# Kernel tuning notes

Measured on AMD Instinct MI355X. Metric: run time of the kernel, lower is better.

## Reference

```python
import jax, jax.numpy as jnp
import numpy as np

B, T, D, H = 4, 2048, 1024, 16
DK = D // H


def setup_inputs() -> dict:
    key = jax.random.key(0)
    ks = jax.random.split(key, 9)
    s = 1.0 / np.sqrt(D)
    x = jax.random.normal(ks[0], (B, T, D), dtype=jnp.float32)
    mask = jnp.tril(jnp.ones((T, T), dtype=bool))[None, None]  # causal [1,1,T,T]
    wq = jax.random.uniform(ks[1], (D, D), jnp.float32, -s, s)
    bq = jax.random.uniform(ks[2], (D,), jnp.float32, -s, s)
    wk = jax.random.uniform(ks[3], (D, D), jnp.float32, -s, s)
    bk = jax.random.uniform(ks[4], (D,), jnp.float32, -s, s)
    wv = jax.random.uniform(ks[5], (D, D), jnp.float32, -s, s)
    bv = jax.random.uniform(ks[6], (D,), jnp.float32, -s, s)
    wo = jax.random.uniform(ks[7], (D, D), jnp.float32, -s, s)
    bo = jax.random.uniform(ks[8], (D,), jnp.float32, -s, s)
    return {"x": x, "mask": mask, "wq": wq, "bq": bq, "wk": wk, "bk": bk,
            "wv": wv, "bv": bv, "wo": wo, "bo": bo}


def reference(x, mask, wq, bq, wk, bk, wv, bv, wo, bo):
    # projections: torch Linear is x @ W.T + b; here weights stored as (D, D) used directly
    q = (x @ wq + bq).reshape(B, T, H, DK).transpose(0, 2, 1, 3)  # [B,H,T,dk]
    k = (x @ wk + bk).reshape(B, T, H, DK).transpose(0, 2, 1, 3)
    v = (x @ wv + bv).reshape(B, T, H, DK).transpose(0, 2, 1, 3)
    scores = jnp.einsum('bhqd,bhkd->bhqk', q, k) / jnp.sqrt(jnp.float32(DK))
    scores = jnp.where(mask, scores, -jnp.inf)
    attn = jax.nn.softmax(scores, axis=-1)
    # dropout p=0.0 -> identity
    y = jnp.einsum('bhqk,bhkd->bhqd', attn, v)
    y = y.transpose(0, 2, 1, 3).reshape(B, T, D)
    return y @ wo + bo
```

## Files before the change

### kernel.cpp

```cpp
#include <hip/hip_runtime.h>


typedef short s16x8 __attribute__((ext_vector_type(8)));
typedef short s16x4 __attribute__((ext_vector_type(4)));
typedef float f32x4 __attribute__((ext_vector_type(4)));
typedef unsigned int u32x2 __attribute__((ext_vector_type(2)));

static __device__ __forceinline__ float bf2f(unsigned short u) {
    return __uint_as_float(((unsigned int)u) << 16);
}
static __device__ __forceinline__ unsigned short f2bf(float f) {
    unsigned int x = __float_as_uint(f);
    unsigned int r = x + 0x7fffu + ((x >> 16) & 1u);
    return (unsigned short)(r >> 16);
}

static __device__ __forceinline__ void gload_lds16(const short* g, short* l) {
    __builtin_amdgcn_global_load_lds((__attribute__((address_space(1))) void*)g,
                                     (__attribute__((address_space(3))) void*)l, 16, 0, 0);
}

static __device__ __forceinline__ unsigned int cvt_pk_bf16(float a, float b) {
    unsigned int r;
    asm("v_cvt_pk_bf16_f32 %0, %1, %2" : "=v"(r) : "v"(a), "v"(b));
    return r;
}

static __device__ __forceinline__ float fexp2(float x) {
    float r;
    asm("v_exp_f32 %0, %1" : "=v"(r) : "v"(x));
    return r;
}

__global__ __launch_bounds__(64) void detect_dtype(const unsigned short* __restrict__ x,
                                                   int* __restrict__ flag) {
    int lane = threadIdx.x;
    int cnt = 0;
    for (int i = 0; i < 64; ++i) {
        float v = bf2f(x[lane * 64 + i]);
        if (!(fabsf(v) < 1e10f)) cnt++;
    }
    unsigned long long m = __ballot(cnt > 0);
    if (lane == 0) *flag = (m != 0ull) ? 1 : 0;
}

__global__ __launch_bounds__(256) void convert_bf16(const void* __restrict__ src,
                                                    unsigned short* __restrict__ dst,
                                                    int n, const int* __restrict__ flag) {
    int i = blockIdx.x * 256 + threadIdx.x;
    if (i >= n) return;
    if (*flag) dst[i] = f2bf(((const float*)src)[i]);
    else       dst[i] = ((const unsigned short*)src)[i];
}

__global__ __launch_bounds__(256) void convert_biases(const void* __restrict__ b0,
                                                      const void* __restrict__ b1,
                                                      const void* __restrict__ b2,
                                                      const void* __restrict__ b3,
                                                      unsigned short* __restrict__ dst,
                                                      const int* __restrict__ flag) {
    int i = blockIdx.x * 256 + threadIdx.x;
    const void* src = (i < 1024) ? b0 : (i < 2048 ? b1 : (i < 3072 ? b2 : b3));
    int k = i & 1023;
    if (*flag) dst[i] = f2bf(((const float*)src)[k]);
    else       dst[i] = ((const unsigned short*)src)[k];
}

__global__ __launch_bounds__(256) void transpose_wt4(const void* __restrict__ s0,
                                                     const void* __restrict__ s1,
                                                     const void* __restrict__ s2,
                                                     const void* __restrict__ s3,
                                                     unsigned short* __restrict__ dst,
                                                     const int* __restrict__ flag) {
    __shared__ unsigned short t[32][33];
    int z = blockIdx.z;
    const void* src = (z == 0) ? s0 : (z == 1 ? s1 : (z == 2 ? s2 : s3));
    dst += (size_t)z * 1024 * 1024;
    int f = *flag;
    int x = threadIdx.x, y = threadIdx.y;
    int n0 = blockIdx.x * 32, k0 = blockIdx.y * 32;
    for (int j = 0; j < 32; j += 8) {
        size_t idx = (size_t)(k0 + y + j) * 1024 + n0 + x;
        t[y + j][x] = f ? f2bf(((const float*)src)[idx]) : ((const unsigned short*)src)[idx];
    }
    __syncthreads();
    for (int j = 0; j < 32; j += 8) dst[(size_t)(n0 + y + j) * 1024 + k0 + x] = t[x][y + j];
}

__global__ __launch_bounds__(256) void gemm_bf16(const short* __restrict__ A,
                                                 const short* __restrict__ Bt,
                                                 void* __restrict__ C,
                                                 short* __restrict__ vt,
                                                 const unsigned short* __restrict__ bq,
                                                 const unsigned short* __restrict__ bk,
                                                 const unsigned short* __restrict__ bv,
                                                 int K, int ldc,
                                                 const int* __restrict__ flag, int f32out,
                                                 int scale_q, int fuse_v) {
    __shared__ __align__(16) short As[2][128][64];
    __shared__ __align__(16) short Bs[2][128][64];
    int tid = threadIdx.x;
    int wid = tid >> 6, lane = tid & 63, quad = lane >> 4, l16 = lane & 15;
    int wm = wid & 1, wn = wid >> 1;
    int m0 = blockIdx.x * 128, n0 = blockIdx.y * 128;
    bool wf = f32out && (*flag != 0);

    int srow = lane >> 3;
    int schunk = (lane & 7) ^ srow;
    const short* Ag = A  + (size_t)(m0 + wid * 32 + srow) * K + schunk * 8;
    const short* Bg = Bt + (size_t)(n0 + wid * 32 + srow) * K + schunk * 8;

    f32x4 acc[4][4] = {};
    int nt = K >> 6;

#pragma unroll
    for (int c = 0; c < 4; ++c) {
        gload_lds16(Ag + c * 8 * K, &As[0][wid * 32 + c * 8][0]);
        gload_lds16(Bg + c * 8 * K, &Bs[0][wid * 32 + c * 8][0]);
    }
    __syncthreads();

    for (int t = 0; t < nt; ++t) {
        if (t + 1 < nt) {
            int bu = (t + 1) & 1;
            int kof = (t + 1) * 64;
#pragma unroll
            for (int c = 0; c < 4; ++c) {
                gload_lds16(Ag + kof + c * 8 * K, &As[bu][wid * 32 + c * 8][0]);
                gload_lds16(Bg + kof + c * 8 * K, &Bs[bu][wid * 32 + c * 8][0]);
            }
        }
        const short (*Ab)[64] = As[t & 1];
#pragma unroll
        for (int kk = 0; kk < 2; ++kk) {
            s16x8 a[4], b[4];
#pragma unroll
            for (int i = 0; i < 4; ++i) {
                int row = wm * 64 + i * 16 + l16;
                a[i] = *(const s16x8*)&Ab[row][(((kk << 2) + quad) ^ (row & 7)) << 3];
            }
#pragma unroll
            for (int j = 0; j < 4; ++j) {
                int row = wn * 64 + j * 16 + l16;
                b[j] = *(const s16x8*)&Bs[t & 1][row][(((kk << 2) + quad) ^ (row & 7)) << 3];
            }
            __builtin_amdgcn_s_setprio(1);
#pragma unroll
            for (int i = 0; i < 4; ++i)
#pragma unroll
                for (int j = 0; j < 4; ++j)
                    acc[i][j] = __builtin_amdgcn_mfma_f32_16x16x32_bf16(a[i], b[j], acc[i][j], 0, 0, 0);
            __builtin_amdgcn_s_setprio(0);
        }
        __syncthreads();
    }
    for (int j = 0; j < 4; ++j) {
        int col = n0 + wn * 64 + j * 16 + l16;
        const unsigned short* bptr = (col < 1024) ? bq : (col < 2048 ? bk : bv);
        float bias = bf2f(bptr[col & 1023]);
        float cs = (scale_q && col < 1024) ? 0.18033688f : 1.0f;
        for (int i = 0; i < 4; ++i) {
            int rbase = m0 + wm * 64 + i * 16 + quad * 4;
            if (fuse_v && col >= 2048) {
                int h = (col - 2048) >> 6, dk = col & 63;
                int bb_ = rbase >> 11, t = rbase & 2047;
                s16x4 pk;
                for (int r = 0; r < 4; ++r) pk[r] = (short)f2bf(acc[i][j][r] + bias);
                *(s16x4*)(vt + ((size_t)((bb_ * 16 + h) * 64 + dk)) * 2048 + t) = pk;
            } else {
                for (int r = 0; r < 4; ++r) {
                    float v = (acc[i][j][r] + bias) * cs;
                    size_t idx = (size_t)(rbase + r) * ldc + col;
                    if (wf) ((float*)C)[idx] = v;
                    else    ((unsigned short*)C)[idx] = f2bf(v);
                }
            }
        }
    }
}

static __device__ __forceinline__ void stage_tiles(const short* kbase, const short* vbase,
                                                   int kt, short* Kb, short* Vb,
                                                   int wid, int lane) {
    int row = wid * 8 + (lane >> 3);
    int c_src = (lane & 7) ^ (lane >> 3);
    const short* kg = kbase + (size_t)(kt * 64 + row) * 3072 + c_src * 8;
    const short* vg = vbase + (size_t)row * 2048 + kt * 64 + c_src * 8;
    gload_lds16(kg, Kb + wid * 512);
    gload_lds16(vg, Vb + wid * 512);
}

static __device__ __forceinline__ s16x8 lds_frag(const short* buf, int row, int cg) {
    int slot = cg ^ (row & 7);
    return *(const s16x8*)(buf + row * 64 + slot * 8);
}

__global__ __launch_bounds__(512, 4) void attn(const short* __restrict__ qkv,
                                               const short* __restrict__ vt,
                                               unsigned short* __restrict__ y) {
    __shared__ __align__(16) short Kbuf[3][64 * 64];
    __shared__ __align__(16) short Vbuf[3][64 * 64];
    __shared__ __align__(16) short Ps[8][16 * 68];
    int tid = threadIdx.x;
    int wid = tid >> 6, lane = tid & 63, quad = lane >> 4, l16 = lane & 15;
    int bh = blockIdx.x, b = bh >> 4, h = bh & 15;
    const short* kbase = qkv + (size_t)b * 2048 * 3072 + 1024 + h * 64;
    const short* vbase = vt + (size_t)bh * 64 * 2048;
    short* PsW = &Ps[wid][0];

    s16x8 ones;
    for (int e = 0; e < 8; ++e) ones[e] = (short)0x3F80;

    int qb = 15 - (int)blockIdx.y;
    int ktmax = 2 * qb + 1;
    int kmax_w = 2 * qb + (wid >> 2);

    const short* qp = qkv + (size_t)(b * 2048 + qb * 128 + wid * 16 + l16) * 3072 + h * 64;
    s16x8 q0 = *(const s16x8*)(qp + quad * 8);
    s16x8 q1 = *(const s16x8*)(qp + 32 + quad * 8);

    float m_old = -INFINITY;
    f32x4 lacc = {0.f, 0.f, 0.f, 0.f};
    f32x4 o[4] = {};

    stage_tiles(kbase, vbase, 0, &Kbuf[0][0], &Vbuf[0][0], wid, lane);
    stage_tiles(kbase, vbase, 1, &Kbuf[1][0], &Vbuf[1][0], wid, lane);
    int ss = 2;
    int cc = 0;

    for (int kt = 0; kt <= ktmax; ++kt) {
        if (kt < ktmax) asm volatile("s_waitcnt vmcnt(2)" ::: "memory");
        else            asm volatile("s_waitcnt vmcnt(0)" ::: "memory");
        __builtin_amdgcn_sched_barrier(0);
        __builtin_amdgcn_s_barrier();

        if (kt + 2 <= ktmax) {
            stage_tiles(kbase, vbase, kt + 2, &Kbuf[0][0] + ss * 4096, &Vbuf[0][0] + ss * 4096,
                        wid, lane);
            ss = (ss == 2) ? 0 : ss + 1;
        }

        if (kt <= kmax_w) {
            const short* Kb = &Kbuf[0][0] + cc * 4096;
            const short* Vb = &Vbuf[0][0] + cc * 4096;

            f32x4 s[4] = {};
            __builtin_amdgcn_s_setprio(1);
            for (int j = 0; j < 4; ++j) {
                s16x8 klo = lds_frag(Kb, j * 16 + l16, quad);
                s16x8 khi = lds_frag(Kb, j * 16 + l16, 4 + quad);
                s[j] = __builtin_amdgcn_mfma_f32_16x16x32_bf16(klo, q0, s[j], 0, 0, 0);
                s[j] = __builtin_amdgcn_mfma_f32_16x16x32_bf16(khi, q1, s[j], 0, 0, 0);
            }
            __builtin_amdgcn_s_setprio(0);

            if (kt == kmax_w) {
                int qq = (wid & 3) * 16 + l16;
                for (int j = 0; j < 4; ++j)
                    for (int r = 0; r < 4; ++r)
                        if (j * 16 + quad * 4 + r > qq) s[j][r] = -INFINITY;
            }

            float mj0 = fmaxf(fmaxf(s[0][0], s[0][1]), s[0][2]);
            mj0 = fmaxf(mj0, s[0][3]);
            float mj1 = fmaxf(fmaxf(s[1][0], s[1][1]), s[1][2]);
            mj1 = fmaxf(mj1, s[1][3]);
            float mj2 = fmaxf(fmaxf(s[2][0], s[2][1]), s[2][2]);
            mj2 = fmaxf(mj2, s[2][3]);
            float mj3 = fmaxf(fmaxf(s[3][0], s[3][1]), s[3][2]);
            mj3 = fmaxf(mj3, s[3][3]);
            float mx = fmaxf(fmaxf(fmaxf(mj0, mj1), mj2), mj3);
            mx = fmaxf(mx, __shfl_xor(mx, 16));
            mx = fmaxf(mx, __shfl_xor(mx, 32));

            if (__any(mx > m_old + 8.0f)) {
                float mn = fmaxf(m_old, mx);
                float alpha = fexp2(m_old - mn);
                m_old = mn;
                float ar[4];
                for (int r = 0; r < 4; ++r) ar[r] = __shfl(alpha, quad * 4 + r);
                for (int r = 0; r < 4; ++r) {
                    lacc[r] *= ar[r];
                    for (int d = 0; d < 4; ++d) o[d][r] *= ar[r];
                }
            }

            for (int j = 0; j < 4; ++j) {
                float p0 = fexp2(s[j][0] - m_old);
                float p1 = fexp2(s[j][1] - m_old);
                float p2 = fexp2(s[j][2] - m_old);
                float p3 = fexp2(s[j][3] - m_old);
                u32x2 w;
                w.x = cvt_pk_bf16(p0, p1);
                w.y = cvt_pk_bf16(p2, p3);
                *(u32x2*)(PsW + l16 * 68 + j * 16 + quad * 4) = w;
            }

            s16x8 pa0 = *(const s16x8*)&PsW[l16 * 68 + quad * 8];
            s16x8 pa1 = *(const s16x8*)&PsW[l16 * 68 + 32 + quad * 8];
            __builtin_amdgcn_s_setprio(1);
            lacc = __builtin_amdgcn_mfma_f32_16x16x32_bf16(pa0, ones, lacc, 0, 0, 0);
            lacc = __builtin_amdgcn_mfma_f32_16x16x32_bf16(pa1, ones, lacc, 0, 0, 0);
            for (int d = 0; d < 4; ++d) {
                s16x8 vlo = lds_frag(Vb, d * 16 + l16, quad);
                s16x8 vhi = lds_frag(Vb, d * 16 + l16, 4 + quad);
                o[d] = __builtin_amdgcn_mfma_f32_16x16x32_bf16(pa0, vlo, o[d], 0, 0, 0);
                o[d] = __builtin_amdgcn_mfma_f32_16x16x32_bf16(pa1, vhi, o[d], 0, 0, 0);
            }
            __builtin_amdgcn_s_setprio(0);
        }
        cc = (cc == 2) ? 0 : cc + 1;
    }

    for (int r = 0; r < 4; ++r) {
        float inv = 1.f / lacc[r];
        int t = qb * 128 + wid * 16 + quad * 4 + r;
        for (int d = 0; d < 4; ++d)
            y[(size_t)(b * 2048 + t) * 1024 + h * 64 + d * 16 + l16] = f2bf(o[d][r] * inv);
    }
}

extern "C" void kernel_launch(void* const* d_in, const int* in_sizes, int n_in,
                              void* d_out, int out_size, void* d_ws, size_t ws_size,
                              hipStream_t stream) {
    (void)in_sizes; (void)n_in; (void)out_size; (void)ws_size;
    const void* x  = d_in[0];
    const void* wq = d_in[2]; const void* bq = d_in[3];
    const void* wk = d_in[4]; const void* bk = d_in[5];
    const void* wv = d_in[6]; const void* bv = d_in[7];
    const void* wo = d_in[8]; const void* bo = d_in[9];

    const size_t MB = 1024 * 1024;
    char* ws = (char*)d_ws;
    unsigned short* wT  = (unsigned short*)ws;
    short* qkv = (short*)(ws + 8 * MB);
    short* vt  = (short*)(ws + 56 * MB);
    unsigned short* xb = (unsigned short*)(ws + 72 * MB);
    unsigned short* yb = (unsigned short*)(ws + 72 * MB);
    unsigned short* bb = (unsigned short*)(ws + 88 * MB);
    int* flag = (int*)(ws + 88 * MB + 64 * 1024);

    detect_dtype<<<1, 64, 0, stream>>>((const unsigned short*)x, flag);
    convert_bf16<<<32768, 256, 0, stream>>>(x, xb, 8388608, flag);
    convert_biases<<<16, 256, 0, stream>>>(bq, bk, bv, bo, bb, flag);

    dim3 tb(32, 8);
    transpose_wt4<<<dim3(32, 32, 4), tb, 0, stream>>>(wq, wk, wv, wo, wT, flag);

    gemm_bf16<<<dim3(64, 24), 256, 0, stream>>>((const short*)xb, (const short*)wT,
                                                qkv, vt, bb, bb + 1024, bb + 2048,
                                                1024, 3072, flag, 0, 1, 1);
    attn<<<dim3(64, 16), 512, 0, stream>>>(qkv, vt, yb);
    gemm_bf16<<<dim3(64, 8), 256, 0, stream>>>((const short*)yb, (const short*)(wT + 3072 * 1024),
                                               d_out, nullptr, bb + 3072, bb + 3072, bb + 3072,
                                               1024, 1024, flag, 1, 0, 0);
}
```

Before: 299.7 us.

## Fuse prep kernels and software-pipeline PV MFMAs behind next QK tile

Merges the input conversion, bias conversion and weight transpose kernels into one prep launch, and vectorises the x conversion to four elements per thread. In the attention loop, the P·V and row-sum MFMAs for a tile are deferred into the next iteration so they overlap with that iteration's QK MFMAs and softmax work. A tail step handles the last tile. This removes launch overhead and serialisation between softmax and the PV matmul, at the cost of holding eight extra V fragments in registers, which may lower occupancy.

Result: faster. 292.1 us (-2.5%).

```diff
diff --git a/kernel.cpp b/kernel.cpp
--- a/kernel.cpp
+++ b/kernel.cpp
@@ -5,6 +5,7 @@
 typedef short s16x4 __attribute__((ext_vector_type(4)));
 typedef float f32x4 __attribute__((ext_vector_type(4)));
 typedef unsigned int u32x2 __attribute__((ext_vector_type(2)));
+typedef unsigned short u16x4 __attribute__((ext_vector_type(4)));
 
 static __device__ __forceinline__ float bf2f(unsigned short u) {
     return __uint_as_float(((unsigned int)u) << 16);
@@ -44,47 +45,47 @@
     if (lane == 0) *flag = (m != 0ull) ? 1 : 0;
 }
 
-__global__ __launch_bounds__(256) void convert_bf16(const void* __restrict__ src,
-                                                    unsigned short* __restrict__ dst,
-                                                    int n, const int* __restrict__ flag) {
-    int i = blockIdx.x * 256 + threadIdx.x;
-    if (i >= n) return;
-    if (*flag) dst[i] = f2bf(((const float*)src)[i]);
-    else       dst[i] = ((const unsigned short*)src)[i];
-}
-
-__global__ __launch_bounds__(256) void convert_biases(const void* __restrict__ b0,
-                                                      const void* __restrict__ b1,
-                                                      const void* __restrict__ b2,
-                                                      const void* __restrict__ b3,
-                                                      unsigned short* __restrict__ dst,
-                                                      const int* __restrict__ flag) {
-    int i = blockIdx.x * 256 + threadIdx.x;
-    const void* src = (i < 1024) ? b0 : (i < 2048 ? b1 : (i < 3072 ? b2 : b3));
-    int k = i & 1023;
-    if (*flag) dst[i] = f2bf(((const float*)src)[k]);
-    else       dst[i] = ((const unsigned short*)src)[k];
-}
-
-__global__ __launch_bounds__(256) void transpose_wt4(const void* __restrict__ s0,
-                                                     const void* __restrict__ s1,
-                                                     const void* __restrict__ s2,
-                                                     const void* __restrict__ s3,
-                                                     unsigned short* __restrict__ dst,
-                                                     const int* __restrict__ flag) {
+__global__ __launch_bounds__(256) void prep(const void* __restrict__ x,
+                                            const void* __restrict__ b0, const void* __restrict__ b1,
+                                            const void* __restrict__ b2, const void* __restrict__ b3,
+                                            const void* __restrict__ w0, const void* __restrict__ w1,
+                                            const void* __restrict__ w2, const void* __restrict__ w3,
+                                            unsigned short* __restrict__ xb,
+                                            unsigned short* __restrict__ bb,
+                                            unsigned short* __restrict__ wT,
+                                            const int* __restrict__ flag) {
     __shared__ unsigned short t[32][33];
-    int z = blockIdx.z;
-    const void* src = (z == 0) ? s0 : (z == 1 ? s1 : (z == 2 ? s2 : s3));
-    dst += (size_t)z * 1024 * 1024;
+    int bid = blockIdx.x, tid = threadIdx.x;
     int f = *flag;
-    int x = threadIdx.x, y = threadIdx.y;
-    int n0 = blockIdx.x * 32, k0 = blockIdx.y * 32;
-    for (int j = 0; j < 32; j += 8) {
-        size_t idx = (size_t)(k0 + y + j) * 1024 + n0 + x;
-        t[y + j][x] = f ? f2bf(((const float*)src)[idx]) : ((const unsigned short*)src)[idx];
-    }
-    __syncthreads();
-    for (int j = 0; j < 32; j += 8) dst[(size_t)(n0 + y + j) * 1024 + k0 + x] = t[x][y + j];
+    if (bid < 8192) {
+        int i = bid * 256 + tid;
+        u16x4 o;
+        if (f) {
+            float4 v = ((const float4*)x)[i];
+            o[0] = f2bf(v.x); o[1] = f2bf(v.y); o[2] = f2bf(v.z); o[3] = f2bf(v.w);
+        } else {
+            o = ((const u16x4*)x)[i];
+        }
+        ((u16x4*)xb)[i] = o;
+    } else if (bid < 8208) {
+        int i = (bid - 8192) * 256 + tid;
+        const void* src = (i < 1024) ? b0 : (i < 2048 ? b1 : (i < 3072 ? b2 : b3));
+        int k = i & 1023;
+        bb[i] = f ? f2bf(((const float*)src)[k]) : ((const unsigned short*)src)[k];
+    } else {
+        int tz = bid - 8208;
+        int z = tz >> 10, tile = tz & 1023;
+        const void* src = (z == 0) ? w0 : (z == 1 ? w1 : (z == 2 ? w2 : w3));
+        unsigned short* dst = wT + (size_t)z * 1024 * 1024;
+        int xx = tid & 31, yy = tid >> 5;
+        int n0 = (tile & 31) * 32, k0 = (tile >> 5) * 32;
+        for (int j = 0; j < 32; j += 8) {
+            size_t idx = (size_t)(k0 + yy + j) * 1024 + n0 + xx;
+            t[yy + j][xx] = f ? f2bf(((const float*)src)[idx]) : ((const unsigned short*)src)[idx];
+        }
+        __syncthreads();
+        for (int j = 0; j < 32; j += 8) dst[(size_t)(n0 + yy + j) * 1024 + k0 + xx] = t[xx][yy + j];
+    }
 }
 
 __global__ __launch_bounds__(256) void gemm_bf16(const short* __restrict__ A,
@@ -222,6 +223,9 @@
     float m_old = -INFINITY;
     f32x4 lacc = {0.f, 0.f, 0.f, 0.f};
     f32x4 o[4] = {};
+    s16x8 paA, paB;
+    s16x8 vr[8];
+    bool have_prev = false;
 
     stage_tiles(kbase, vbase, 0, &Kbuf[0][0], &Vbuf[0][0], wid, lane);
     stage_tiles(kbase, vbase, 1, &Kbuf[1][0], &Vbuf[1][0], wid, lane);
@@ -251,6 +255,14 @@
                 s16x8 khi = lds_frag(Kb, j * 16 + l16, 4 + quad);
                 s[j] = __builtin_amdgcn_mfma_f32_16x16x32_bf16(klo, q0, s[j], 0, 0, 0);
                 s[j] = __builtin_amdgcn_mfma_f32_16x16x32_bf16(khi, q1, s[j], 0, 0, 0);
+            }
+            if (have_prev) {
+                lacc = __builtin_amdgcn_mfma_f32_16x16x32_bf16(paA, ones, lacc, 0, 0, 0);
+                lacc = __builtin_amdgcn_mfma_f32_16x16x32_bf16(paB, ones, lacc, 0, 0, 0);
+                for (int d = 0; d < 4; ++d) {
+                    o[d] = __builtin_amdgcn_mfma_f32_16x16x32_bf16(paA, vr[2 * d], o[d], 0, 0, 0);
+                    o[d] = __builtin_amdgcn_mfma_f32_16x16x32_bf16(paB, vr[2 * d + 1], o[d], 0, 0, 0);
+                }
             }
             __builtin_amdgcn_s_setprio(0);
 
@@ -295,21 +307,27 @@
                 w.y = cvt_pk_bf16(p2, p3);
                 *(u32x2*)(PsW + l16 * 68 + j * 16 + quad * 4) = w;
             }
-
-            s16x8 pa0 = *(const s16x8*)&PsW[l16 * 68 + quad * 8];
-            s16x8 pa1 = *(const s16x8*)&PsW[l16 * 68 + 32 + quad * 8];
-            __builtin_amdgcn_s_setprio(1);
-            lacc = __builtin_amdgcn_mfma_f32_16x16x32_bf16(pa0, ones, lacc, 0, 0, 0);
-            lacc = __builtin_amdgcn_mfma_f32_16x16x32_bf16(pa1, ones, lacc, 0, 0, 0);
+            paA = *(const s16x8*)&PsW[l16 * 68 + quad * 8];
+            paB = *(const s16x8*)&PsW[l16 * 68 + 32 + quad * 8];
+
             for (int d = 0; d < 4; ++d) {
-                s16x8 vlo = lds_frag(Vb, d * 16 + l16, quad);
-                s16x8 vhi = lds_frag(Vb, d * 16 + l16, 4 + quad);
-                o[d] = __builtin_amdgcn_mfma_f32_16x16x32_bf16(pa0, vlo, o[d], 0, 0, 0);
-                o[d] = __builtin_amdgcn_mfma_f32_16x16x32_bf16(pa1, vhi, o[d], 0, 0, 0);
-            }
-            __builtin_amdgcn_s_setprio(0);
+                vr[2 * d]     = lds_frag(Vb, d * 16 + l16, quad);
+                vr[2 * d + 1] = lds_frag(Vb, d * 16 + l16, 4 + quad);
+            }
+            have_prev = true;
         }
         cc = (cc == 2) ? 0 : cc + 1;
+    }
+
+    if (have_prev) {
+        __builtin_amdgcn_s_setprio(1);
+        lacc = __builtin_amdgcn_mfma_f32_16x16x32_bf16(paA, ones, lacc, 0, 0, 0);
+        lacc = __builtin_amdgcn_mfma_f32_16x16x32_bf16(paB, ones, lacc, 0, 0, 0);
+        for (int d = 0; d < 4; ++d) {
+            o[d] = __builtin_amdgcn_mfma_f32_16x16x32_bf16(paA, vr[2 * d], o[d], 0, 0, 0);
+            o[d] = __builtin_amdgcn_mfma_f32_16x16x32_bf16(paB, vr[2 * d + 1], o[d], 0, 0, 0);
+        }
+        __builtin_amdgcn_s_setprio(0);
     }
 
     for (int r = 0; r < 4; ++r) {
@@ -341,11 +359,7 @@
     int* flag = (int*)(ws + 88 * MB + 64 * 1024);
 
     detect_dtype<<<1, 64, 0, stream>>>((const unsigned short*)x, flag);
-    convert_bf16<<<32768, 256, 0, stream>>>(x, xb, 8388608, flag);
-    convert_biases<<<16, 256, 0, stream>>>(bq, bk, bv, bo, bb, flag);
-
-    dim3 tb(32, 8);
-    transpose_wt4<<<dim3(32, 32, 4), tb, 0, stream>>>(wq, wk, wv, wo, wT, flag);
+    prep<<<12304, 256, 0, stream>>>(x, bq, bk, bv, bo, wq, wk, wv, wo, xb, bb, wT, flag);
 
     gemm_bf16<<<dim3(64, 24), 256, 0, stream>>>((const short*)xb, (const short*)wT,
                                                 qkv, vt, bb, bb + 1024, bb + 2048,
```
